# Performance work log

Measured on AMD Instinct MI355X. Metric: run time of the kernel, lower is better.

## Reference

```python
import jax, jax.numpy as jnp
import numpy as np

B, S, D_IN, D_EMB = 16, 8192, 256, 256
LEVELS = 8  # pywt default max level for db1 with signal length 256: log2(256)
INV_SQRT2 = np.float32(1.0 / np.sqrt(2.0))


def haar_wavedec_concat(x, levels):
    """Multi-level Haar (db1) DWT along last axis; returns coeffs concatenated
    in pywt order [cA_L, cD_L, ..., cD_1]. Assumes last dim = 2**levels,
    so 'symmetric' padding is a no-op (filter length 2, even lengths).
    pywt db1 convention: cA[k]=(x[2k]+x[2k+1])/sqrt2, cD[k]=(x[2k]-x[2k+1])/sqrt2.
    """
    details = []
    a = x
    for _ in range(levels):
        even = a[..., ::2]
        odd = a[..., 1::2]
        details.append((even - odd) * INV_SQRT2)
        a = (even + odd) * INV_SQRT2
    return jnp.concatenate([a] + details[::-1], axis=-1)


def setup_inputs() -> dict:
    key = jax.random.key(0)
    k_x, k_w, k_b = jax.random.split(key, 3)
    x = jax.random.normal(k_x, (B, S, D_IN), dtype=jnp.float32)
    # nn.Linear(input_dim, embed_dim): W is (embed_dim, input_dim)
    bound = np.float32(1.0 / np.sqrt(D_IN))
    W = jax.random.uniform(k_w, (D_EMB, D_IN), dtype=jnp.float32, minval=-bound, maxval=bound)
    b = jax.random.uniform(k_b, (D_EMB,), dtype=jnp.float32, minval=-bound, maxval=bound)
    return {"x": x, "W": W, "b": b}


def reference(x, W, b):
    coeffs = haar_wavedec_concat(x, LEVELS)  # (B, S, D_IN)
    # concatenated coeff length == D_IN exactly, so no pad/trim (matches original no-op branch)
    return jnp.einsum('bsd,ed->bse', coeffs, W) + b
```

## Files before the change

### kernel.cpp

```cpp
#include <hip/hip_runtime.h>
#include <hip/hip_bf16.h>

typedef short short8 __attribute__((ext_vector_type(8)));
typedef float f32x4 __attribute__((ext_vector_type(4)));

__device__ __forceinline__ unsigned short f2bf(float f) {
  union { float f; unsigned u; } v; v.f = f;
  unsigned u = v.u;
  unsigned r = (u + 0x7FFFu + ((u >> 16) & 1u)) >> 16;
  return (unsigned short)r;
}

__global__ void haar_pack(const float* __restrict__ W, unsigned short* __restrict__ Wp) {
  const int e = blockIdx.x;
  const int k = threadIdx.x;
  const float* row = W + e * 256;
  const float wgt[9] = {0.f,
    0.70710678118654752f, 0.5f, 0.35355339059327376f, 0.25f,
    0.17677669529663688f, 0.125f, 0.08838834764831844f, 0.0625f};
  float acc = row[0] * 0.0625f;
#pragma unroll
  for (int l = 1; l <= 8; ++l) {
    float g = wgt[l];
    float s = ((k >> (l - 1)) & 1) ? -g : g;
    acc += row[(1 << (8 - l)) + (k >> l)] * s;
  }
  const int nblk = e >> 4, lr = e & 15;
  const int kk = k >> 5, win = k & 31, lhi = win >> 3, j = win & 7;
  const int lane = lhi * 16 + lr;
  Wp[(((nblk * 8 + kk) * 64 + lane) << 3) + j] = f2bf(acc);
}

#define NTILES 16
#define BM 32

#define BARRIER_LGKM() do { \
    __builtin_amdgcn_sched_barrier(0); \
    asm volatile("s_waitcnt lgkmcnt(0)" ::: "memory"); \
    __builtin_amdgcn_s_barrier(); \
    __builtin_amdgcn_sched_barrier(0); \
  } while (0)

__global__ __launch_bounds__(512, 1) void wemb_gemm(
    const float* __restrict__ x, const unsigned short* __restrict__ Wp,
    const float* __restrict__ bias, float* __restrict__ out) {
  __shared__ char al[2][16384];
  const int tid = threadIdx.x;
  const int w = tid >> 6, lane = tid & 63;
  const int wm = w >> 2, wn = w & 3;
  const int lr = lane & 15, lhi = lane >> 4;

  short8 Bf[8][4];
#pragma unroll
  for (int kk = 0; kk < 8; ++kk)
#pragma unroll
    for (int n = 0; n < 4; ++n)
      Bf[kk][n] = *(const short8*)(Wp + ((((wn * 4 + n) * 8 + kk) * 64 + lane) << 3));

  f32x4 bias4[4];
#pragma unroll
  for (int n = 0; n < 4; ++n)
    bias4[n] = *(const f32x4*)(bias + wn * 64 + n * 16 + lhi * 4);

  const long tile0 = (long)blockIdx.x * NTILES;
  float4 pfA[4], pfB[4];

  {
    const float4* s0 = (const float4*)(x + tile0 * (BM * 256));
    float4 t0[4];
#pragma unroll
    for (int i = 0; i < 4; ++i) t0[i] = s0[i * 512 + tid];
    const float4* s1 = (const float4*)(x + (tile0 + 1) * (BM * 256));
#pragma unroll
    for (int i = 0; i < 4; ++i) pfA[i] = s1[i * 512 + tid];
#pragma unroll
    for (int i = 0; i < 4; ++i) {
      int f = i * 512 + tid;
      int row = f >> 6, colb = (f & 63) * 8;
      ushort4 p;
      p.x = __bfloat16_as_ushort(__float2bfloat16(t0[i].x));
      p.y = __bfloat16_as_ushort(__float2bfloat16(t0[i].y));
      p.z = __bfloat16_as_ushort(__float2bfloat16(t0[i].z));
      p.w = __bfloat16_as_ushort(__float2bfloat16(t0[i].w));
      *(ushort4*)(al[0] + row * 512 + (colb ^ ((row & 7) << 4))) = p;
    }
  }
  BARRIER_LGKM();

#define STEP(IT, CUR, NXT, PFU, PFL)                                          \
  {                                                                           \
    const long tt = tile0 + (IT);                                             \
    if ((IT) + 2 < NTILES) {                                                  \
      const float4* src = (const float4*)(x + (tt + 2) * (BM * 256));         \
      _Pragma("unroll")                                                       \
      for (int i = 0; i < 4; ++i) PFL[i] = src[i * 512 + tid];                \
    }                                                                         \
    f32x4 acc[4];                                                             \
    _Pragma("unroll")                                                         \
    for (int n = 0; n < 4; ++n) acc[n] = (f32x4){0.f, 0.f, 0.f, 0.f};         \
    _Pragma("unroll")                                                         \
    for (int kk = 0; kk < 8; ++kk) {                                          \
      const int arow = wm * 16 + lr;                                          \
      const int colb = (kk * 32 + lhi * 8) * 2;                               \
      short8 a = *(const short8*)((CUR) + arow * 512 +                        \
                                  (colb ^ ((arow & 7) << 4)));                \
      _Pragma("unroll")                                                       \
      for (int n = 0; n < 4; ++n)                                             \
        acc[n] = __builtin_amdgcn_mfma_f32_16x16x32_bf16(Bf[kk][n], a,        \
                                                         acc[n], 0, 0, 0);    \
    }                                                                         \
    {                                                                         \
      float* orow = out + (tt * BM + wm * 16 + lr) * 256 + wn * 64 + lhi * 4; \
      _Pragma("unroll")                                                       \
      for (int n = 0; n < 4; ++n) {                                           \
        f32x4 v = acc[n] + bias4[n];                                          \
        *(f32x4*)(orow + n * 16) = v;                                         \
      }                                                                       \
    }                                                                         \
    if ((IT) + 1 < NTILES) {                                                  \
      _Pragma("unroll")                                                       \
      for (int i = 0; i < 4; ++i) {                                           \
        int f = i * 512 + tid;                                                \
        int row = f >> 6, colb = (f & 63) * 8;                                \
        ushort4 p;                                                            \
        p.x = __bfloat16_as_ushort(__float2bfloat16(PFU[i].x));               \
        p.y = __bfloat16_as_ushort(__float2bfloat16(PFU[i].y));               \
        p.z = __bfloat16_as_ushort(__float2bfloat16(PFU[i].z));               \
        p.w = __bfloat16_as_ushort(__float2bfloat16(PFU[i].w));               \
        *(ushort4*)((NXT) + row * 512 + (colb ^ ((row & 7) << 4))) = p;       \
      }                                                                       \
      BARRIER_LGKM();                                                         \
    }                                                                         \
  }

#pragma unroll 1
  for (int ip = 0; ip < NTILES / 2; ++ip) {
    const int it0 = ip * 2;
    STEP(it0,     al[0], al[1], pfA, pfB);
    STEP(it0 + 1, al[1], al[0], pfB, pfA);
  }
#undef STEP
}

extern "C" void kernel_launch(void* const* d_in, const int* in_sizes, int n_in,
                              void* d_out, int out_size, void* d_ws, size_t ws_size,
                              hipStream_t stream) {
  const float* x = (const float*)d_in[0];
  const float* W = (const float*)d_in[1];
  const float* b = (const float*)d_in[2];
  float* out = (float*)d_out;
  unsigned short* Wp = (unsigned short*)d_ws;

  haar_pack<<<256, 256, 0, stream>>>(W, Wp);

  const int grid = (out_size / 256) / (BM * NTILES);
  wemb_gemm<<<grid, 512, 0, stream>>>(x, Wp, b, out);
}
```

Measured before the change: 59.93 us.

## Load x fragments directly into registers, dropping LDS staging and barriers

Removes the shared-memory staging of x tiles, so each wave loads its MFMA A-operand straight from global memory into registers and converts it to bf16 in place. Waves now all share the same 16 rows and split the 256 output columns 8 ways, and the bias is folded into the accumulator init. This removes the LDS writes, reads and block barriers, but each wave re-reads the same x rows, so the block issues eight times the global/L1 traffic for x.

```diff
diff --git a/kernel.cpp b/kernel.cpp
--- a/kernel.cpp
+++ b/kernel.cpp
@@ -31,115 +31,96 @@
   Wp[(((nblk * 8 + kk) * 64 + lane) << 3) + j] = f2bf(acc);
 }
 
-#define NTILES 16
-#define BM 32
-
-#define BARRIER_LGKM() do { \
-    __builtin_amdgcn_sched_barrier(0); \
-    asm volatile("s_waitcnt lgkmcnt(0)" ::: "memory"); \
-    __builtin_amdgcn_s_barrier(); \
-    __builtin_amdgcn_sched_barrier(0); \
-  } while (0)
+#define NT 16
 
 __global__ __launch_bounds__(512, 1) void wemb_gemm(
     const float* __restrict__ x, const unsigned short* __restrict__ Wp,
     const float* __restrict__ bias, float* __restrict__ out) {
-  __shared__ char al[2][16384];
   const int tid = threadIdx.x;
-  const int w = tid >> 6, lane = tid & 63;
-  const int wm = w >> 2, wn = w & 3;
+  const int wn = tid >> 6;
+  const int lane = tid & 63;
   const int lr = lane & 15, lhi = lane >> 4;
 
-  short8 Bf[8][4];
+  short8 Bf[8][2];
 #pragma unroll
   for (int kk = 0; kk < 8; ++kk)
 #pragma unroll
-    for (int n = 0; n < 4; ++n)
-      Bf[kk][n] = *(const short8*)(Wp + ((((wn * 4 + n) * 8 + kk) * 64 + lane) << 3));
+    for (int n = 0; n < 2; ++n)
+      Bf[kk][n] = *(const short8*)(Wp + ((((wn * 2 + n) * 8 + kk) * 64 + lane) << 3));
+#pragma unroll
+  for (int kk = 0; kk < 8; ++kk)
+#pragma unroll
+    for (int n = 0; n < 2; ++n)
+      asm volatile("" : "+v"(Bf[kk][n]));
 
-  f32x4 bias4[4];
+  f32x4 bias4[2];
 #pragma unroll
-  for (int n = 0; n < 4; ++n)
-    bias4[n] = *(const f32x4*)(bias + wn * 64 + n * 16 + lhi * 4);
+  for (int n = 0; n < 2; ++n)
+    bias4[n] = *(const f32x4*)(bias + wn * 32 + n * 16 + lhi * 4);
 
-  const long tile0 = (long)blockIdx.x * NTILES;
-  float4 pfA[4], pfB[4];
+  const long row0 = (long)blockIdx.x * (16 * NT) + lr;
+  const float* xbase = x + row0 * 256 + lhi * 8;
 
-  {
-    const float4* s0 = (const float4*)(x + tile0 * (BM * 256));
-    float4 t0[4];
+  float4 PA[8], PB[8], Q[8];
+
 #pragma unroll
-    for (int i = 0; i < 4; ++i) t0[i] = s0[i * 512 + tid];
-    const float4* s1 = (const float4*)(x + (tile0 + 1) * (BM * 256));
-#pragma unroll
-    for (int i = 0; i < 4; ++i) pfA[i] = s1[i * 512 + tid];
-#pragma unroll
-    for (int i = 0; i < 4; ++i) {
-      int f = i * 512 + tid;
-      int row = f >> 6, colb = (f & 63) * 8;
-      ushort4 p;
-      p.x = __bfloat16_as_ushort(__float2bfloat16(t0[i].x));
-      p.y = __bfloat16_as_ushort(__float2bfloat16(t0[i].y));
-      p.z = __bfloat16_as_ushort(__float2bfloat16(t0[i].z));
-      p.w = __bfloat16_as_ushort(__float2bfloat16(t0[i].w));
-      *(ushort4*)(al[0] + row * 512 + (colb ^ ((row & 7) << 4))) = p;
-    }
+  for (int i = 0; i < 8; ++i)
+    PA[i] = *(const float4*)(xbase + (i >> 1) * 32 + (i & 1) * 4);
+
+#define CVT8(FR, LO, HI) { \
+    union { short8 s; unsigned short h[8]; } u_;                              \
+    u_.h[0] = __bfloat16_as_ushort(__float2bfloat16((LO).x));                 \
+    u_.h[1] = __bfloat16_as_ushort(__float2bfloat16((LO).y));                 \
+    u_.h[2] = __bfloat16_as_ushort(__float2bfloat16((LO).z));                 \
+    u_.h[3] = __bfloat16_as_ushort(__float2bfloat16((LO).w));                 \
+    u_.h[4] = __bfloat16_as_ushort(__float2bfloat16((HI).x));                 \
+    u_.h[5] = __bfloat16_as_ushort(__float2bfloat16((HI).y));                 \
+    u_.h[6] = __bfloat16_as_ushort(__float2bfloat16((HI).z));                 \
+    u_.h[7] = __bfloat16_as_ushort(__float2bfloat16((HI).w));                 \
+    FR = u_.s;                                                                \
   }
-  BARRIER_LGKM();
 
-#define STEP(IT, CUR, NXT, PFU, PFL)                                          \
+#define STEP(T, PC, PN)                                                       \
   {                                                                           \
-    const long tt = tile0 + (IT);                                             \
-    if ((IT) + 2 < NTILES) {                                                  \
-      const float4* src = (const float4*)(x + (tt + 2) * (BM * 256));         \
+    const float* xr = xbase + (long)(T) * (16 * 256);                         \
+    _Pragma("unroll")                                                         \
+    for (int i = 0; i < 8; ++i)                  \
+      Q[i] = *(const float4*)(xr + 128 + (i >> 1) * 32 + (i & 1) * 4);        \
+    if ((T) + 1 < NT) {                          \
       _Pragma("unroll")                                                       \
-      for (int i = 0; i < 4; ++i) PFL[i] = src[i * 512 + tid];                \
+      for (int i = 0; i < 8; ++i)                                             \
+        PN[i] = *(const float4*)(xr + 16 * 256 + (i >> 1) * 32 + (i & 1) * 4);\
     }                                                                         \
-    f32x4 acc[4];                                                             \
+    f32x4 acc[2];                                                             \
+    acc[0] = bias4[0]; acc[1] = bias4[1];                                     \
     _Pragma("unroll")                                                         \
-    for (int n = 0; n < 4; ++n) acc[n] = (f32x4){0.f, 0.f, 0.f, 0.f};         \
-    _Pragma("unroll")                                                         \
-    for (int kk = 0; kk < 8; ++kk) {                                          \
-      const int arow = wm * 16 + lr;                                          \
-      const int colb = (kk * 32 + lhi * 8) * 2;                               \
-      short8 a = *(const short8*)((CUR) + arow * 512 +                        \
-                                  (colb ^ ((arow & 7) << 4)));                \
+    for (int kk = 0; kk < 4; ++kk) {                                          \
+      short8 fr; CVT8(fr, PC[2 * kk], PC[2 * kk + 1]);                        \
       _Pragma("unroll")                                                       \
-      for (int n = 0; n < 4; ++n)                                             \
-        acc[n] = __builtin_amdgcn_mfma_f32_16x16x32_bf16(Bf[kk][n], a,        \
+      for (int n = 0; n < 2; ++n)                                             \
+        acc[n] = __builtin_amdgcn_mfma_f32_16x16x32_bf16(Bf[kk][n], fr,       \
                                                          acc[n], 0, 0, 0);    \
     }                                                                         \
-    {                                                                         \
-      float* orow = out + (tt * BM + wm * 16 + lr) * 256 + wn * 64 + lhi * 4; \
+    _Pragma("unroll")                                                         \
+    for (int kk = 4; kk < 8; ++kk) {                                          \
+      short8 fr; CVT8(fr, Q[2 * (kk - 4)], Q[2 * (kk - 4) + 1]);              \
       _Pragma("unroll")                                                       \
-      for (int n = 0; n < 4; ++n) {                                           \
-        f32x4 v = acc[n] + bias4[n];                                          \
-        *(f32x4*)(orow + n * 16) = v;                                         \
-      }                                                                       \
+      for (int n = 0; n < 2; ++n)                                             \
+        acc[n] = __builtin_amdgcn_mfma_f32_16x16x32_bf16(Bf[kk][n], fr,       \
+                                                         acc[n], 0, 0, 0);    \
     }                                                                         \
-    if ((IT) + 1 < NTILES) {                                                  \
-      _Pragma("unroll")                                                       \
-      for (int i = 0; i < 4; ++i) {                                           \
-        int f = i * 512 + tid;                                                \
-        int row = f >> 6, colb = (f & 63) * 8;                                \
-        ushort4 p;                                                            \
-        p.x = __bfloat16_as_ushort(__float2bfloat16(PFU[i].x));               \
-        p.y = __bfloat16_as_ushort(__float2bfloat16(PFU[i].y));               \
-        p.z = __bfloat16_as_ushort(__float2bfloat16(PFU[i].z));               \
-        p.w = __bfloat16_as_ushort(__float2bfloat16(PFU[i].w));               \
-        *(ushort4*)((NXT) + row * 512 + (colb ^ ((row & 7) << 4))) = p;       \
-      }                                                                       \
-      BARRIER_LGKM();                                                         \
-    }                                                                         \
+    float* orow = out + (row0 + (T) * 16) * 256 + wn * 32 + lhi * 4;          \
+    *(f32x4*)(orow) = acc[0];                                                 \
+    *(f32x4*)(orow + 16) = acc[1];                                            \
   }
 
 #pragma unroll 1
-  for (int ip = 0; ip < NTILES / 2; ++ip) {
-    const int it0 = ip * 2;
-    STEP(it0,     al[0], al[1], pfA, pfB);
-    STEP(it0 + 1, al[1], al[0], pfB, pfA);
+  for (int tp = 0; tp < NT / 2; ++tp) {
+    STEP(tp * 2,     PA, PB);
+    STEP(tp * 2 + 1, PB, PA);
   }
 #undef STEP
+#undef CVT8
 }
 
 extern "C" void kernel_launch(void* const* d_in, const int* in_sizes, int n_in,
@@ -153,6 +134,6 @@
 
   haar_pack<<<256, 256, 0, stream>>>(W, Wp);
 
-  const int grid = (out_size / 256) / (BM * NTILES);
+  const int grid = (out_size / 256) / (16 * NT);
   wemb_gemm<<<grid, 512, 0, stream>>>(x, Wp, b, out);
 }
```

Measured after the change: 131.2 us. 119% more time.
